# Kernel tuning notes

Measured on AMD Instinct MI355X. Metric: run time of the kernel, lower is better.

Reference implementation:

```python
import jax, jax.numpy as jnp
import numpy as np

DEPTH = 15  # complete binary tree, N = 2**DEPTH - 1 nodes, heap layout


def setup_inputs() -> dict:
    key = jax.random.key(0)
    ks = jax.random.split(key, 9)
    D, H = 512, 512
    N = 2 ** DEPTH - 1
    s = 0.02
    return {
        "x": jax.random.normal(ks[0], (N, D), jnp.float32),
        "Wi": jax.random.normal(ks[1], (H, D + H), jnp.float32) * s,
        "bi": jax.random.normal(ks[2], (H,), jnp.float32) * s,
        "Wf": jax.random.normal(ks[3], (H, D + H), jnp.float32) * s,
        "bf": jax.random.normal(ks[4], (H,), jnp.float32) * s,
        "Wo": jax.random.normal(ks[5], (H, D + H), jnp.float32) * s,
        "bo": jax.random.normal(ks[6], (H,), jnp.float32) * s,
        "Wu": jax.random.normal(ks[7], (H, D + H), jnp.float32) * s,
        "bu": jax.random.normal(ks[8], (H,), jnp.float32) * s,
    }


def _tree_lstm(x, Wi, bi, Wf, bf, Wo, bo, Wu, bu):
    # Child-Sum Tree-LSTM on a complete binary tree in heap layout.
    # Levels processed bottom-up; each level is fully batched.
    N, D = x.shape
    H = Wi.shape[0]
    sig, tanh = jax.nn.sigmoid, jnp.tanh
    h = jnp.zeros((N, H), x.dtype)
    c = jnp.zeros((N, H), x.dtype)
    for lvl in range(DEPTH - 1, -1, -1):
        start = 2 ** lvl - 1
        cnt = 2 ** lvl
        xl = x[start:start + cnt]  # [cnt, D]
        if lvl == DEPTH - 1:
            # leaf_forward: h_children = 0, no forget gates
            xh = jnp.concatenate([xl, jnp.zeros((cnt, H), x.dtype)], axis=1)
            i = sig(xh @ Wi.T + bi)
            o = sig(xh @ Wo.T + bo)
            u = tanh(xh @ Wu.T + bu)
            cl = i * u
        else:
            cs = 2 * start + 1  # first child index of this level
            ch = h[cs:cs + 2 * cnt].reshape(cnt, 2, H)
            cc = c[cs:cs + 2 * cnt].reshape(cnt, 2, H)
            h_l, h_r = ch[:, 0], ch[:, 1]
            hsum = h_l + h_r  # child-sum
            xh = jnp.concatenate([xl, hsum], axis=1)
            i = sig(xh @ Wi.T + bi)
            o = sig(xh @ Wo.T + bo)
            u = tanh(xh @ Wu.T + bu)
            # per-child forget gates: f_k = sigmoid(Wf @ [x; h_k] + bf)
            f_l = sig(jnp.concatenate([xl, h_l], axis=1) @ Wf.T + bf)
            f_r = sig(jnp.concatenate([xl, h_r], axis=1) @ Wf.T + bf)
            cl = i * u + f_l * cc[:, 0] + f_r * cc[:, 1]
        hl = o * tanh(cl)
        h = h.at[start:start + cnt].set(hl)
        c = c.at[start:start + cnt].set(cl)
    return h[0], c[0]  # root (h, c), matching torch forward's return


def reference(x, Wi, bi, Wf, bf, Wo, bo, Wu, bu):
    return _tree_lstm(x, Wi, bi, Wf, bf, Wo, bo, Wu, bu)
```

## Files before the change

### kernel.cpp

```cpp
#include <hip/hip_runtime.h>

typedef __attribute__((ext_vector_type(8))) short bf16x8;
typedef __attribute__((ext_vector_type(4))) float f32x4;

#define HHE 512

__device__ __forceinline__ unsigned short rne_bf16(float f) {
    union { float f; unsigned u; } v; v.f = f;
    unsigned r = v.u + 0x7FFFu + ((v.u >> 16) & 1u);
    return (unsigned short)(r >> 16);
}
__device__ __forceinline__ float bf2f(unsigned short s) {
    union { unsigned u; float f; } v; v.u = ((unsigned)s) << 16; return v.f;
}
__device__ __forceinline__ float sigf(float v)   { return 1.0f / (1.0f + __expf(-v)); }
__device__ __forceinline__ float tanhf_(float v) { return 2.0f / (1.0f + __expf(-2.0f * v)) - 1.0f; }

#define MFMA16(a, b, c) __builtin_amdgcn_mfma_f32_16x16x32_bf16(a, b, c, 0, 0, 0)

#define GLOAD_LDS16(g, l) \
    __builtin_amdgcn_global_load_lds((const __attribute__((address_space(1))) void*)(g), \
                                     (__attribute__((address_space(3))) void*)(l), 16, 0, 0)

__global__ __launch_bounds__(256) void prep(
    const float* __restrict__ x,
    const float* __restrict__ Wi, const float* __restrict__ Wf,
    const float* __restrict__ Wo, const float* __restrict__ Wu,
    unsigned short* __restrict__ xb, unsigned short* __restrict__ wp)
{
    const int b = blockIdx.x;
    if (b < 1024) {
        int t    = b * 256 + threadIdx.x;
        int lane = t & 63;
        int fid  = t >> 6;
        int ks   = fid & 31;
        int jt   = (fid >> 5) & 31;
        int g    = fid >> 10;
        const float* W = (g == 0) ? Wi : (g == 1) ? Wf : (g == 2) ? Wo : Wu;
        int row = jt * 16 + (lane & 15);
        int col = ks * 32 + (lane >> 4) * 8;
        const float* src = W + (size_t)row * 1024 + col;
        float4 f0 = *(const float4*)(src);
        float4 f1 = *(const float4*)(src + 4);
        uint4 o;
        o.x = (unsigned)rne_bf16(f0.x) | ((unsigned)rne_bf16(f0.y) << 16);
        o.y = (unsigned)rne_bf16(f0.z) | ((unsigned)rne_bf16(f0.w) << 16);
        o.z = (unsigned)rne_bf16(f1.x) | ((unsigned)rne_bf16(f1.y) << 16);
        o.w = (unsigned)rne_bf16(f1.z) | ((unsigned)rne_bf16(f1.w) << 16);
        ((uint4*)wp)[t] = o;
    } else {
        size_t idx = (size_t)(b - 1024) * 256 + threadIdx.x;
        if (idx >= 2097088) return;
        const float4* p = (const float4*)x + idx * 2;
        float4 f0 = p[0], f1 = p[1];
        uint4 o;
        o.x = (unsigned)rne_bf16(f0.x) | ((unsigned)rne_bf16(f0.y) << 16);
        o.y = (unsigned)rne_bf16(f0.z) | ((unsigned)rne_bf16(f0.w) << 16);
        o.z = (unsigned)rne_bf16(f1.x) | ((unsigned)rne_bf16(f1.y) << 16);
        o.w = (unsigned)rne_bf16(f1.z) | ((unsigned)rne_bf16(f1.w) << 16);
        ((uint4*)xb)[idx] = o;
    }
}

__global__ __launch_bounds__(256) void leaf_v3(
    const unsigned short* __restrict__ xb, const unsigned short* __restrict__ wp,
    const float* __restrict__ bi, const float* __restrict__ bo, const float* __restrict__ bu,
    unsigned short* __restrict__ hw, unsigned short* __restrict__ cw,
    unsigned short* __restrict__ hso,
    int start, int cnt)
{
    __shared__ __align__(16) unsigned short SH[2 * 2048];

    const int tid  = threadIdx.x;
    const int lane = tid & 63;
    const int wv   = tid >> 6;
    const int q    = lane >> 4;
    const int ln   = lane & 15;
    const int wm   = wv & 1;
    const int wj   = wv >> 1;
    const int mb   = blockIdx.x * 64;
    const int jt0  = blockIdx.y * 4 + wj * 2;

    const int srow   = lane >> 2;
    const int gchunk = (lane & 3) ^ ((lane >> 3) & 3);
    const int stage_row = mb + wv * 16 + srow;
    const int rdoff = ((q ^ ((ln >> 1) & 3)) * 8);

    const unsigned short* wpl = wp + (size_t)lane * 8;

    f32x4 zero = {0.f, 0.f, 0.f, 0.f};
    f32x4 acc_i[2][2], acc_o[2][2], acc_u[2][2];
    #pragma unroll
    for (int t = 0; t < 2; ++t)
        #pragma unroll
        for (int ji = 0; ji < 2; ++ji) {
            acc_i[t][ji] = zero; acc_o[t][ji] = zero; acc_u[t][ji] = zero;
        }

    bf16x8 WA[3][2], WB[3][2];

    auto loadW = [&](bf16x8 (&W)[3][2], int ksabs) {
        #pragma unroll
        for (int g = 0; g < 3; ++g) {
            const int gg = (g == 0) ? 0 : (g + 1);
            #pragma unroll
            for (int ji = 0; ji < 2; ++ji)
                W[g][ji] = *(const bf16x8*)(wpl + ((size_t)((gg * 32 + jt0 + ji) * 32 + ksabs)) * 512);
        }
    };

    loadW(WA, 0);
    {
        const unsigned short* g = xb + (size_t)(start + stage_row) * HHE + gchunk * 8;
        GLOAD_LDS16(g, &SH[0 * 2048 + wv * 512]);
    }
    __syncthreads();

    auto body = [&](int ks, bf16x8 (&WU)[3][2], bf16x8 (&WP)[3][2], int prefks) {
        const int cur = ks & 1;
        if (ks < 15) {
            const unsigned short* g = xb + (size_t)(start + stage_row) * HHE + (ks + 1) * 32 + gchunk * 8;
            GLOAD_LDS16(g, &SH[(cur ^ 1) * 2048 + wv * 512]);
        }
        loadW(WP, prefks);
        bf16x8 a0 = *(const bf16x8*)&SH[cur * 2048 + (wm * 32 + 0 + ln) * 32 + rdoff];
        bf16x8 a1 = *(const bf16x8*)&SH[cur * 2048 + (wm * 32 + 16 + ln) * 32 + rdoff];
        #pragma unroll
        for (int ji = 0; ji < 2; ++ji) {
            acc_i[0][ji] = MFMA16(a0, WU[0][ji], acc_i[0][ji]);
            acc_i[1][ji] = MFMA16(a1, WU[0][ji], acc_i[1][ji]);
            acc_o[0][ji] = MFMA16(a0, WU[1][ji], acc_o[0][ji]);
            acc_o[1][ji] = MFMA16(a1, WU[1][ji], acc_o[1][ji]);
            acc_u[0][ji] = MFMA16(a0, WU[2][ji], acc_u[0][ji]);
            acc_u[1][ji] = MFMA16(a1, WU[2][ji], acc_u[1][ji]);
        }
        __syncthreads();
    };

    for (int kk = 0; kk < 8; ++kk) {
        body(2 * kk,     WA, WB, 2 * kk + 1);
        body(2 * kk + 1, WB, WA, (kk == 7) ? 15 : 2 * kk + 2);
    }

    #pragma unroll
    for (int ji = 0; ji < 2; ++ji) {
        const int jj = (jt0 + ji) * 16 + ln;
        const float bij = bi[jj], boj = bo[jj], buj = bu[jj];
        #pragma unroll
        for (int t = 0; t < 2; ++t) {
            const int n0 = mb + wm * 32 + t * 16 + q * 4;
            float hv[4];
            #pragma unroll
            for (int r = 0; r < 4; ++r) {
                const int node = n0 + r;
                float gi = sigf(acc_i[t][ji][r] + bij);
                float go = sigf(acc_o[t][ji][r] + boj);
                float gu = tanhf_(acc_u[t][ji][r] + buj);
                float cnv = gi * gu;
                float hnv = go * tanhf_(cnv);
                hv[r] = hnv;
                size_t oix = (size_t)node * HHE + jj;
                hw[oix] = rne_bf16(hnv);
                cw[oix] = rne_bf16(cnv);
            }
            hso[(size_t)(n0 >> 1) * HHE + jj]       = rne_bf16(hv[0] + hv[1]);
            hso[(size_t)((n0 >> 1) + 1) * HHE + jj] = rne_bf16(hv[2] + hv[3]);
        }
    }
}

__global__ __launch_bounds__(256) void level_v3(
    const unsigned short* __restrict__ xb, const unsigned short* __restrict__ wp,
    const float* __restrict__ bi, const float* __restrict__ bfv,
    const float* __restrict__ bo, const float* __restrict__ bu,
    const unsigned short* __restrict__ hc, const unsigned short* __restrict__ cc,
    const unsigned short* __restrict__ hs,
    unsigned short* __restrict__ hw, unsigned short* __restrict__ cw,
    unsigned short* __restrict__ hso,
    int start, int cnt)
{
    __shared__ __align__(16) unsigned short SH[2 * 3 * 2048];

    const int tid  = threadIdx.x;
    const int lane = tid & 63;
    const int wv   = tid >> 6;
    const int q    = lane >> 4;
    const int ln   = lane & 15;
    const int wm   = wv & 1;
    const int wj   = wv >> 1;
    const int mb   = blockIdx.x * 64;
    const int jt0  = blockIdx.y * 4 + wj * 2;

    const int srow   = lane >> 2;
    const int gchunk = (lane & 3) ^ ((lane >> 3) & 3);
    const int stage_row = mb + wv * 16 + srow;
    const int rdoff = ((q ^ ((ln >> 1) & 3)) * 8);

    const unsigned short* wpl = wp + (size_t)lane * 8;

    f32x4 zero = {0.f, 0.f, 0.f, 0.f};
    f32x4 acc_i[2][2], acc_f[2][2], acc_o[2][2], acc_u[2][2];
    #pragma unroll
    for (int t = 0; t < 2; ++t)
        #pragma unroll
        for (int ji = 0; ji < 2; ++ji) {
            acc_i[t][ji] = zero; acc_f[t][ji] = zero;
            acc_o[t][ji] = zero; acc_u[t][ji] = zero;
        }

    bf16x8 WA[4][2], WB[4][2];

    auto loadW = [&](bf16x8 (&W)[4][2], int ksabs) {
        #pragma unroll
        for (int g = 0; g < 4; ++g)
            #pragma unroll
            for (int ji = 0; ji < 2; ++ji)
                W[g][ji] = *(const bf16x8*)(wpl + ((size_t)((g * 32 + jt0 + ji) * 32 + ksabs)) * 512);
    };

    loadW(WA, 0);
    {
        const unsigned short* g = xb + (size_t)(start + stage_row) * HHE + gchunk * 8;
        GLOAD_LDS16(g, &SH[(0 * 3 + 0) * 2048 + wv * 512]);
    }
    __syncthreads();

    auto p1_body = [&](int ks, bf16x8 (&WU)[4][2], bf16x8 (&WP)[4][2], int prefks) {
        const int cur = ks & 1;
        if (ks < 15) {
            const unsigned short* g = xb + (size_t)(start + stage_row) * HHE + (ks + 1) * 32 + gchunk * 8;
            GLOAD_LDS16(g, &SH[((cur ^ 1) * 3 + 0) * 2048 + wv * 512]);
        }
        loadW(WP, prefks);
        bf16x8 a0 = *(const bf16x8*)&SH[(cur * 3 + 0) * 2048 + (wm * 32 + 0 + ln) * 32 + rdoff];
        bf16x8 a1 = *(const bf16x8*)&SH[(cur * 3 + 0) * 2048 + (wm * 32 + 16 + ln) * 32 + rdoff];
        #pragma unroll
        for (int ji = 0; ji < 2; ++ji) {
            acc_i[0][ji] = MFMA16(a0, WU[0][ji], acc_i[0][ji]);
            acc_i[1][ji] = MFMA16(a1, WU[0][ji], acc_i[1][ji]);
            acc_f[0][ji] = MFMA16(a0, WU[1][ji], acc_f[0][ji]);
            acc_f[1][ji] = MFMA16(a1, WU[1][ji], acc_f[1][ji]);
            acc_o[0][ji] = MFMA16(a0, WU[2][ji], acc_o[0][ji]);
            acc_o[1][ji] = MFMA16(a1, WU[2][ji], acc_o[1][ji]);
            acc_u[0][ji] = MFMA16(a0, WU[3][ji], acc_u[0][ji]);
            acc_u[1][ji] = MFMA16(a1, WU[3][ji], acc_u[1][ji]);
        }
        __syncthreads();
    };

    for (int kk = 0; kk < 8; ++kk) {
        p1_body(2 * kk,     WA, WB, 2 * kk + 1);
        p1_body(2 * kk + 1, WB, WA, (kk == 7) ? 16 : 2 * kk + 2);
    }

    f32x4 acc_fl[2][2], acc_fr[2][2];
    #pragma unroll
    for (int t = 0; t < 2; ++t)
        #pragma unroll
        for (int ji = 0; ji < 2; ++ji) { acc_fl[t][ji] = acc_f[t][ji]; acc_fr[t][ji] = acc_f[t][ji]; }

    {
        const unsigned short* gs = hs + (size_t)stage_row * HHE + gchunk * 8;
        const unsigned short* gl = hc + ((size_t)(2 * stage_row)) * HHE + gchunk * 8;
        GLOAD_LDS16(gs, &SH[(0 * 3 + 0) * 2048 + wv * 512]);
        GLOAD_LDS16(gl, &SH[(0 * 3 + 1) * 2048 + wv * 512]);
        GLOAD_LDS16(gl + HHE, &SH[(0 * 3 + 2) * 2048 + wv * 512]);
    }
    __syncthreads();

    auto p2_body = [&](int ks, bf16x8 (&WU)[4][2], bf16x8 (&WP)[4][2], int prefks) {
        const int cur = ks & 1;
        if (ks < 15) {
            const unsigned short* gs = hs + (size_t)stage_row * HHE + (ks + 1) * 32 + gchunk * 8;
            const unsigned short* gl = hc + ((size_t)(2 * stage_row)) * HHE + (ks + 1) * 32 + gchunk * 8;
            GLOAD_LDS16(gs, &SH[((cur ^ 1) * 3 + 0) * 2048 + wv * 512]);
            GLOAD_LDS16(gl, &SH[((cur ^ 1) * 3 + 1) * 2048 + wv * 512]);
            GLOAD_LDS16(gl + HHE, &SH[((cur ^ 1) * 3 + 2) * 2048 + wv * 512]);
        }
        loadW(WP, prefks);
        bf16x8 s0 = *(const bf16x8*)&SH[(cur * 3 + 0) * 2048 + (wm * 32 + 0 + ln) * 32 + rdoff];
        bf16x8 s1 = *(const bf16x8*)&SH[(cur * 3 + 0) * 2048 + (wm * 32 + 16 + ln) * 32 + rdoff];
        bf16x8 l0 = *(const bf16x8*)&SH[(cur * 3 + 1) * 2048 + (wm * 32 + 0 + ln) * 32 + rdoff];
        bf16x8 l1 = *(const bf16x8*)&SH[(cur * 3 + 1) * 2048 + (wm * 32 + 16 + ln) * 32 + rdoff];
        bf16x8 r0 = *(const bf16x8*)&SH[(cur * 3 + 2) * 2048 + (wm * 32 + 0 + ln) * 32 + rdoff];
        bf16x8 r1 = *(const bf16x8*)&SH[(cur * 3 + 2) * 2048 + (wm * 32 + 16 + ln) * 32 + rdoff];
        #pragma unroll
        for (int ji = 0; ji < 2; ++ji) {
            acc_i[0][ji]  = MFMA16(s0, WU[0][ji], acc_i[0][ji]);
            acc_i[1][ji]  = MFMA16(s1, WU[0][ji], acc_i[1][ji]);
            acc_o[0][ji]  = MFMA16(s0, WU[2][ji], acc_o[0][ji]);
            acc_o[1][ji]  = MFMA16(s1, WU[2][ji], acc_o[1][ji]);
            acc_u[0][ji]  = MFMA16(s0, WU[3][ji], acc_u[0][ji]);
            acc_u[1][ji]  = MFMA16(s1, WU[3][ji], acc_u[1][ji]);
            acc_fl[0][ji] = MFMA16(l0, WU[1][ji], acc_fl[0][ji]);
            acc_fl[1][ji] = MFMA16(l1, WU[1][ji], acc_fl[1][ji]);
            acc_fr[0][ji] = MFMA16(r0, WU[1][ji], acc_fr[0][ji]);
            acc_fr[1][ji] = MFMA16(r1, WU[1][ji], acc_fr[1][ji]);
        }
        __syncthreads();
    };

    for (int kk = 0; kk < 8; ++kk) {
        p2_body(2 * kk,     WA, WB, 16 + 2 * kk + 1);
        p2_body(2 * kk + 1, WB, WA, (kk == 7) ? 31 : 16 + 2 * kk + 2);
    }

    #pragma unroll
    for (int ji = 0; ji < 2; ++ji) {
        const int jj = (jt0 + ji) * 16 + ln;
        const float bij = bi[jj], bfj = bfv[jj], boj = bo[jj], buj = bu[jj];
        #pragma unroll
        for (int t = 0; t < 2; ++t) {
            const int n0 = mb + wm * 32 + t * 16 + q * 4;
            float hv[4];
            #pragma unroll
            for (int r = 0; r < 4; ++r) {
                const int node = n0 + r;
                size_t cix = (size_t)(2 * node) * HHE + jj;
                float cl = bf2f(cc[cix]);
                float cr = bf2f(cc[cix + HHE]);
                float gi  = sigf(acc_i[t][ji][r] + bij);
                float gfl = sigf(acc_fl[t][ji][r] + bfj);
                float gfr = sigf(acc_fr[t][ji][r] + bfj);
                float go  = sigf(acc_o[t][ji][r] + boj);
                float gu  = tanhf_(acc_u[t][ji][r] + buj);
                float cnv = gi * gu + gfl * cl + gfr * cr;
                float hnv = go * tanhf_(cnv);
                hv[r] = hnv;
                size_t oix = (size_t)node * HHE + jj;
                hw[oix] = rne_bf16(hnv);
                cw[oix] = rne_bf16(cnv);
            }
            hso[(size_t)(n0 >> 1) * HHE + jj]       = rne_bf16(hv[0] + hv[1]);
            hso[(size_t)((n0 >> 1) + 1) * HHE + jj] = rne_bf16(hv[2] + hv[3]);
        }
    }
}

__global__ __launch_bounds__(256) void level_sm(
    const unsigned short* __restrict__ xb, const unsigned short* __restrict__ wp,
    const float* __restrict__ bi, const float* __restrict__ bfv,
    const float* __restrict__ bo, const float* __restrict__ bu,
    const unsigned short* __restrict__ hc, const unsigned short* __restrict__ cc,
    const unsigned short* __restrict__ hs,
    unsigned short* __restrict__ hw, unsigned short* __restrict__ cw,
    unsigned short* __restrict__ hso,
    float* __restrict__ f32out,
    int start, int cnt)
{
    const int tid  = threadIdx.x;
    const int lane = tid & 63;
    const int wv   = tid >> 6;
    const int quad = lane >> 4;
    const int ln   = lane & 15;
    const int mb   = blockIdx.x * 32;
    const int jt   = blockIdx.y * 4 + wv;
    const int j    = jt * 16 + ln;

    int row[2];
    #pragma unroll
    for (int t = 0; t < 2; ++t) {
        int r = mb + t * 16 + ln;
        row[t] = (r < cnt) ? r : (cnt - 1);
    }
    const unsigned short* ax[2];
    #pragma unroll
    for (int t = 0; t < 2; ++t) ax[t] = xb + (size_t)(start + row[t]) * HHE + quad * 8;

    const unsigned short* bw[4];
    #pragma unroll
    for (int g = 0; g < 4; ++g) bw[g] = wp + ((size_t)(g * 32 + jt) * 32) * 512 + lane * 8;

    f32x4 zero = {0.f, 0.f, 0.f, 0.f};
    f32x4 acc_i[2], acc_f[2], acc_o[2], acc_u[2];
    #pragma unroll
    for (int t = 0; t < 2; ++t) { acc_i[t] = zero; acc_f[t] = zero; acc_o[t] = zero; acc_u[t] = zero; }

    #pragma unroll 4
    for (int ks = 0; ks < 16; ++ks) {
        bf16x8 a[2];
        #pragma unroll
        for (int t = 0; t < 2; ++t) { a[t] = *(const bf16x8*)ax[t]; ax[t] += 32; }
        bf16x8 b0 = *(const bf16x8*)bw[0]; bw[0] += 512;
        bf16x8 b1 = *(const bf16x8*)bw[1]; bw[1] += 512;
        bf16x8 b2 = *(const bf16x8*)bw[2]; bw[2] += 512;
        bf16x8 b3 = *(const bf16x8*)bw[3]; bw[3] += 512;
        #pragma unroll
        for (int t = 0; t < 2; ++t) {
            acc_i[t] = MFMA16(a[t], b0, acc_i[t]);
            acc_f[t] = MFMA16(a[t], b1, acc_f[t]);
            acc_o[t] = MFMA16(a[t], b2, acc_o[t]);
            acc_u[t] = MFMA16(a[t], b3, acc_u[t]);
        }
    }

    f32x4 acc_fl[2], acc_fr[2];
    #pragma unroll
    for (int t = 0; t < 2; ++t) { acc_fl[t] = acc_f[t]; acc_fr[t] = acc_f[t]; }

    const unsigned short* as[2];
    const unsigned short* al[2];
    const unsigned short* ar[2];
    #pragma unroll
    for (int t = 0; t < 2; ++t) {
        as[t] = hs + (size_t)row[t] * HHE + quad * 8;
        al[t] = hc + (size_t)(2 * row[t]) * HHE + quad * 8;
        ar[t] = al[t] + HHE;
    }

    #pragma unroll 4
    for (int ks = 0; ks < 16; ++ks) {
        bf16x8 b0 = *(const bf16x8*)bw[0]; bw[0] += 512;
        bf16x8 b1 = *(const bf16x8*)bw[1]; bw[1] += 512;
        bf16x8 b2 = *(const bf16x8*)bw[2]; bw[2] += 512;
        bf16x8 b3 = *(const bf16x8*)bw[3]; bw[3] += 512;
        bf16x8 s[2];
        #pragma unroll
        for (int t = 0; t < 2; ++t) { s[t] = *(const bf16x8*)as[t]; as[t] += 32; }
        #pragma unroll
        for (int t = 0; t < 2; ++t) {
            acc_i[t] = MFMA16(s[t], b0, acc_i[t]);
            acc_o[t] = MFMA16(s[t], b2, acc_o[t]);
            acc_u[t] = MFMA16(s[t], b3, acc_u[t]);
        }
        bf16x8 l[2];
        #pragma unroll
        for (int t = 0; t < 2; ++t) { l[t] = *(const bf16x8*)al[t]; al[t] += 32; }
        #pragma unroll
        for (int t = 0; t < 2; ++t) acc_fl[t] = MFMA16(l[t], b1, acc_fl[t]);
        bf16x8 rr[2];
        #pragma unroll
        for (int t = 0; t < 2; ++t) { rr[t] = *(const bf16x8*)ar[t]; ar[t] += 32; }
        #pragma unroll
        for (int t = 0; t < 2; ++t) acc_fr[t] = MFMA16(rr[t], b1, acc_fr[t]);
    }

    const float bij = bi[j], bfj = bfv[j], boj = bo[j], buj = bu[j];
    #pragma unroll
    for (int t = 0; t < 2; ++t) {
        const int n0 = mb + t * 16 + quad * 4;
        float hv[4];
        #pragma unroll
        for (int r = 0; r < 4; ++r) {
            const int node = n0 + r;
            const int ncl  = (node < cnt) ? node : (cnt - 1);
            size_t cix = (size_t)(2 * ncl) * HHE + j;
            float cl = bf2f(cc[cix]);
            float cr = bf2f(cc[cix + HHE]);
            float gi  = sigf(acc_i[t][r] + bij);
            float gfl = sigf(acc_fl[t][r] + bfj);
            float gfr = sigf(acc_fr[t][r] + bfj);
            float go  = sigf(acc_o[t][r] + boj);
            float gu  = tanhf_(acc_u[t][r] + buj);
            float cnv = gi * gu + gfl * cl + gfr * cr;
            float hnv = go * tanhf_(cnv);
            hv[r] = hnv;
            if (node < cnt) {
                size_t oix = (size_t)node * HHE + j;
                hw[oix] = rne_bf16(hnv);
                cw[oix] = rne_bf16(cnv);
                if (f32out) {
                    f32out[(size_t)node * 1024 + j]       = hnv;
                    f32out[(size_t)node * 1024 + 512 + j] = cnv;
                }
            }
        }
        if (n0 + 1 < cnt) hso[(size_t)(n0 >> 1) * HHE + j]       = rne_bf16(hv[0] + hv[1]);
        if (n0 + 3 < cnt) hso[(size_t)((n0 >> 1) + 1) * HHE + j] = rne_bf16(hv[2] + hv[3]);
    }
}

extern "C" void kernel_launch(void* const* d_in, const int* in_sizes, int n_in,
                              void* d_out, int out_size, void* d_ws, size_t ws_size,
                              hipStream_t stream) {
    const float* x  = (const float*)d_in[0];
    const float* Wi = (const float*)d_in[1];
    const float* bi = (const float*)d_in[2];
    const float* Wf = (const float*)d_in[3];
    const float* bf = (const float*)d_in[4];
    const float* Wo = (const float*)d_in[5];
    const float* bo = (const float*)d_in[6];
    const float* Wu = (const float*)d_in[7];
    const float* bu = (const float*)d_in[8];
    float* out = (float*)d_out;

    unsigned short* xb  = (unsigned short*)d_ws;
    unsigned short* wp  = xb  + 16776704;
    unsigned short* hA  = wp  + 2097152;
    unsigned short* hB  = hA  + 8388608;
    unsigned short* hs1 = hB  + 4194304;
    unsigned short* hs2 = hs1 + 4194304;
    unsigned short* cA  = hs2 + 2097152;
    unsigned short* cB  = cA  + 8388608;

    prep<<<9216, 256, 0, stream>>>(x, Wi, Wf, Wo, Wu, xb, wp);

    leaf_v3<<<dim3(256, 8), 256, 0, stream>>>(xb, wp, bi, bo, bu, hA, cA, hs1, 16383, 16384);

    for (int lvl = 13; lvl >= 6; --lvl) {
        int cnt   = 1 << lvl;
        int start = cnt - 1;
        const unsigned short *hc, *cc, *hs;
        unsigned short *hw, *cw, *hso;
        if (lvl & 1) { hc = hA; cc = cA; hs = hs1; hw = hB; cw = cB; hso = hs2; }
        else         { hc = hB; cc = cB; hs = hs2; hw = hA; cw = cA; hso = hs1; }
        level_v3<<<dim3(cnt / 64, 8), 256, 0, stream>>>(xb, wp, bi, bf, bo, bu,
                                                        hc, cc, hs, hw, cw, hso, start, cnt);
    }

    for (int lvl = 5; lvl >= 0; --lvl) {
        int cnt   = 1 << lvl;
        int start = cnt - 1;
        const unsigned short *hc, *cc, *hs;
        unsigned short *hw, *cw, *hso;
        if (lvl & 1) { hc = hA; cc = cA; hs = hs1; hw = hB; cw = cB; hso = hs2; }
        else         { hc = hB; cc = cB; hs = hs2; hw = hA; cw = cA; hso = hs1; }
        float* f32out = (lvl == 0) ? out : nullptr;
        level_sm<<<dim3((cnt + 31) / 32, 8), 256, 0, stream>>>(xb, wp, bi, bf, bo, bu,
                                                               hc, cc, hs, hw, cw, hso, f32out,
                                                               start, cnt);
    }
}
```

Baseline: 564.2 us.

## Triple-buffer LDS staging with one barrier per k-step and manual vmcnt waits

Switches the leaf and level kernels from double-buffered LDS staging with two __syncthreads per k-step to a three-slot ring buffer. Each step now has a single s_barrier, preceded by explicit s_waitcnt vmcnt counts that let the prefetch of the next slice stay in flight. s_setprio also raises wave priority around the MFMA block. The goal is to remove a barrier per step and overlap global-to-LDS loads with matrix math, at the cost of more LDS and hand-tuned vmcnt counts that break if the compiler reorders or adds memory ops. The leaf kernel computes its slot index with an odd nested expression instead of a modulo.

```diff
diff --git a/kernel.cpp b/kernel.cpp
--- a/kernel.cpp
+++ b/kernel.cpp
@@ -69,7 +69,7 @@
     unsigned short* __restrict__ hso,
     int start, int cnt)
 {
-    __shared__ __align__(16) unsigned short SH[2 * 2048];
+    __shared__ __align__(16) unsigned short SH[3 * 2048];
 
     const int tid  = threadIdx.x;
     const int lane = tid & 63;
@@ -114,17 +114,22 @@
         const unsigned short* g = xb + (size_t)(start + stage_row) * HHE + gchunk * 8;
         GLOAD_LDS16(g, &SH[0 * 2048 + wv * 512]);
     }
-    __syncthreads();
 
     auto body = [&](int ks, bf16x8 (&WU)[3][2], bf16x8 (&WP)[3][2], int prefks) {
-        const int cur = ks & 1;
+        loadW(WP, prefks);
         if (ks < 15) {
+            int nxt = ks + 1; nxt -= (nxt >= 3) ? ((nxt >= 6) ? ((nxt >= 9) ? ((nxt >= 12) ? ((nxt >= 15) ? 15 : 12) : 9) : 6) : 3) : 0;
             const unsigned short* g = xb + (size_t)(start + stage_row) * HHE + (ks + 1) * 32 + gchunk * 8;
-            GLOAD_LDS16(g, &SH[(cur ^ 1) * 2048 + wv * 512]);
-        }
-        loadW(WP, prefks);
+            GLOAD_LDS16(g, &SH[nxt * 2048 + wv * 512]);
+            asm volatile("s_waitcnt vmcnt(7)" ::: "memory");
+        } else {
+            asm volatile("s_waitcnt vmcnt(6)" ::: "memory");
+        }
+        __builtin_amdgcn_s_barrier();
+        int cur = ks % 3;
         bf16x8 a0 = *(const bf16x8*)&SH[cur * 2048 + (wm * 32 + 0 + ln) * 32 + rdoff];
         bf16x8 a1 = *(const bf16x8*)&SH[cur * 2048 + (wm * 32 + 16 + ln) * 32 + rdoff];
+        __builtin_amdgcn_s_setprio(1);
         #pragma unroll
         for (int ji = 0; ji < 2; ++ji) {
             acc_i[0][ji] = MFMA16(a0, WU[0][ji], acc_i[0][ji]);
@@ -134,7 +139,7 @@
             acc_u[0][ji] = MFMA16(a0, WU[2][ji], acc_u[0][ji]);
             acc_u[1][ji] = MFMA16(a1, WU[2][ji], acc_u[1][ji]);
         }
-        __syncthreads();
+        __builtin_amdgcn_s_setprio(0);
     };
 
     for (int kk = 0; kk < 8; ++kk) {
@@ -179,7 +184,7 @@
     unsigned short* __restrict__ hso,
     int start, int cnt)
 {
-    __shared__ __align__(16) unsigned short SH[2 * 3 * 2048];
+    __shared__ __align__(16) unsigned short SH[9 * 2048];
 
     const int tid  = threadIdx.x;
     const int lane = tid & 63;
@@ -223,17 +228,22 @@
         const unsigned short* g = xb + (size_t)(start + stage_row) * HHE + gchunk * 8;
         GLOAD_LDS16(g, &SH[(0 * 3 + 0) * 2048 + wv * 512]);
     }
-    __syncthreads();
 
     auto p1_body = [&](int ks, bf16x8 (&WU)[4][2], bf16x8 (&WP)[4][2], int prefks) {
-        const int cur = ks & 1;
+        loadW(WP, prefks);
         if (ks < 15) {
+            int nxt = (ks + 1) % 3;
             const unsigned short* g = xb + (size_t)(start + stage_row) * HHE + (ks + 1) * 32 + gchunk * 8;
-            GLOAD_LDS16(g, &SH[((cur ^ 1) * 3 + 0) * 2048 + wv * 512]);
-        }
-        loadW(WP, prefks);
+            GLOAD_LDS16(g, &SH[(nxt * 3 + 0) * 2048 + wv * 512]);
+            asm volatile("s_waitcnt vmcnt(9)" ::: "memory");
+        } else {
+            asm volatile("s_waitcnt vmcnt(8)" ::: "memory");
+        }
+        __builtin_amdgcn_s_barrier();
+        int cur = ks % 3;
         bf16x8 a0 = *(const bf16x8*)&SH[(cur * 3 + 0) * 2048 + (wm * 32 + 0 + ln) * 32 + rdoff];
         bf16x8 a1 = *(const bf16x8*)&SH[(cur * 3 + 0) * 2048 + (wm * 32 + 16 + ln) * 32 + rdoff];
+        __builtin_amdgcn_s_setprio(1);
         #pragma unroll
         for (int ji = 0; ji < 2; ++ji) {
             acc_i[0][ji] = MFMA16(a0, WU[0][ji], acc_i[0][ji]);
@@ -245,7 +255,7 @@
             acc_u[0][ji] = MFMA16(a0, WU[3][ji], acc_u[0][ji]);
             acc_u[1][ji] = MFMA16(a1, WU[3][ji], acc_u[1][ji]);
         }
-        __syncthreads();
+        __builtin_amdgcn_s_setprio(0);
     };
 
     for (int kk = 0; kk < 8; ++kk) {
@@ -259,6 +269,7 @@
         #pragma unroll
         for (int ji = 0; ji < 2; ++ji) { acc_fl[t][ji] = acc_f[t][ji]; acc_fr[t][ji] = acc_f[t][ji]; }
 
+    __builtin_amdgcn_s_barrier();
     {
         const unsigned short* gs = hs + (size_t)stage_row * HHE + gchunk * 8;
         const unsigned short* gl = hc + ((size_t)(2 * stage_row)) * HHE + gchunk * 8;
@@ -266,24 +277,29 @@
         GLOAD_LDS16(gl, &SH[(0 * 3 + 1) * 2048 + wv * 512]);
         GLOAD_LDS16(gl + HHE, &SH[(0 * 3 + 2) * 2048 + wv * 512]);
     }
-    __syncthreads();
 
     auto p2_body = [&](int ks, bf16x8 (&WU)[4][2], bf16x8 (&WP)[4][2], int prefks) {
-        const int cur = ks & 1;
+        loadW(WP, prefks);
         if (ks < 15) {
+            int nxt = (ks + 1) % 3;
             const unsigned short* gs = hs + (size_t)stage_row * HHE + (ks + 1) * 32 + gchunk * 8;
             const unsigned short* gl = hc + ((size_t)(2 * stage_row)) * HHE + (ks + 1) * 32 + gchunk * 8;
-            GLOAD_LDS16(gs, &SH[((cur ^ 1) * 3 + 0) * 2048 + wv * 512]);
-            GLOAD_LDS16(gl, &SH[((cur ^ 1) * 3 + 1) * 2048 + wv * 512]);
-            GLOAD_LDS16(gl + HHE, &SH[((cur ^ 1) * 3 + 2) * 2048 + wv * 512]);
-        }
-        loadW(WP, prefks);
+            GLOAD_LDS16(gs, &SH[(nxt * 3 + 0) * 2048 + wv * 512]);
+            GLOAD_LDS16(gl, &SH[(nxt * 3 + 1) * 2048 + wv * 512]);
+            GLOAD_LDS16(gl + HHE, &SH[(nxt * 3 + 2) * 2048 + wv * 512]);
+            asm volatile("s_waitcnt vmcnt(11)" ::: "memory");
+        } else {
+            asm volatile("s_waitcnt vmcnt(8)" ::: "memory");
+        }
+        __builtin_amdgcn_s_barrier();
+        int cur = ks % 3;
         bf16x8 s0 = *(const bf16x8*)&SH[(cur * 3 + 0) * 2048 + (wm * 32 + 0 + ln) * 32 + rdoff];
         bf16x8 s1 = *(const bf16x8*)&SH[(cur * 3 + 0) * 2048 + (wm * 32 + 16 + ln) * 32 + rdoff];
         bf16x8 l0 = *(const bf16x8*)&SH[(cur * 3 + 1) * 2048 + (wm * 32 + 0 + ln) * 32 + rdoff];
         bf16x8 l1 = *(const bf16x8*)&SH[(cur * 3 + 1) * 2048 + (wm * 32 + 16 + ln) * 32 + rdoff];
         bf16x8 r0 = *(const bf16x8*)&SH[(cur * 3 + 2) * 2048 + (wm * 32 + 0 + ln) * 32 + rdoff];
         bf16x8 r1 = *(const bf16x8*)&SH[(cur * 3 + 2) * 2048 + (wm * 32 + 16 + ln) * 32 + rdoff];
+        __builtin_amdgcn_s_setprio(1);
         #pragma unroll
         for (int ji = 0; ji < 2; ++ji) {
             acc_i[0][ji]  = MFMA16(s0, WU[0][ji], acc_i[0][ji]);
@@ -297,7 +313,7 @@
             acc_fr[0][ji] = MFMA16(r0, WU[1][ji], acc_fr[0][ji]);
             acc_fr[1][ji] = MFMA16(r1, WU[1][ji], acc_fr[1][ji]);
         }
-        __syncthreads();
+        __builtin_amdgcn_s_setprio(0);
     };
 
     for (int kk = 0; kk < 8; ++kk) {
```

Result: no change. 574.3 us (+1.8%).

## Fuse top seven tree levels into one persistent kernel with grid barrier

Applied to the files above, without the earlier changes.

Replaces the seven separate launches for levels 6 to 0 with one persistent kernel of 32 blocks. Each block owns 16 hidden columns and keeps its slice of all four gate weight matrices in LDS for every level. Levels are separated by a global atomic spin barrier whose counter is reset in the prep kernel. This removes launch overhead and repeated weight loads on the small, latency-bound top levels, but it relies on all 32 blocks being co-resident and on device-scope fences to make each level's outputs visible to the next.

```diff
diff --git a/kernel.cpp b/kernel.cpp
--- a/kernel.cpp
+++ b/kernel.cpp
@@ -26,11 +26,13 @@
     const float* __restrict__ x,
     const float* __restrict__ Wi, const float* __restrict__ Wf,
     const float* __restrict__ Wo, const float* __restrict__ Wu,
-    unsigned short* __restrict__ xb, unsigned short* __restrict__ wp)
+    unsigned short* __restrict__ xb, unsigned short* __restrict__ wp,
+    int* __restrict__ bar)
 {
     const int b = blockIdx.x;
     if (b < 1024) {
         int t    = b * 256 + threadIdx.x;
+        if (bar && t == 0) *bar = 0;
         int lane = t & 63;
         int fid  = t >> 6;
         int ks   = fid & 31;
@@ -470,6 +472,133 @@
     }
 }
 
+#define TAIL_NBLK 32
+
+__device__ __forceinline__ void tailbar(int* bar, int target) {
+    __syncthreads();
+    if (threadIdx.x == 0) {
+        __threadfence();
+        __hip_atomic_fetch_add(bar, 1, __ATOMIC_RELAXED, __HIP_MEMORY_SCOPE_AGENT);
+        while (__hip_atomic_load(bar, __ATOMIC_RELAXED, __HIP_MEMORY_SCOPE_AGENT) < target)
+            __builtin_amdgcn_s_sleep(2);
+        __threadfence();
+    }
+    __syncthreads();
+}
+
+__global__ __launch_bounds__(256) void tail_fused(
+    const unsigned short* __restrict__ xb, const unsigned short* __restrict__ wp,
+    const float* __restrict__ bi, const float* __restrict__ bfv,
+    const float* __restrict__ bo, const float* __restrict__ bu,
+    unsigned short* __restrict__ hA, unsigned short* __restrict__ cA,
+    unsigned short* __restrict__ hB, unsigned short* __restrict__ cB,
+    unsigned short* __restrict__ hs1, unsigned short* __restrict__ hs2,
+    float* __restrict__ out, int* __restrict__ bar)
+{
+    __shared__ __align__(16) unsigned short WL[128 * 512];
+
+    const int tid  = threadIdx.x;
+    const int lane = tid & 63;
+    const int wv   = tid >> 6;
+    const int quad = lane >> 4;
+    const int ln   = lane & 15;
+    const int jt   = blockIdx.x;
+    const int j    = jt * 16 + ln;
+    const int wl   = lane * 8;
+
+    #pragma unroll
+    for (int i = 0; i < 32; ++i) {
+        int f = i * 4 + wv;
+        const unsigned short* src = wp + ((size_t)(((f >> 5) * 32 + jt) * 32 + (f & 31))) * 512 + lane * 8;
+        GLOAD_LDS16(src, &WL[f * 512]);
+    }
+    __syncthreads();
+
+    const float bij = bi[j], bfj = bfv[j], boj = bo[j], buj = bu[j];
+
+    int k = 0;
+    for (int lvl = 6; lvl >= 0; --lvl) {
+        const int cnt = 1 << lvl;
+        const int start = cnt - 1;
+        const unsigned short *hc, *cc, *hs;
+        unsigned short *hw, *cw, *hso;
+        if (lvl & 1) { hc = hA; cc = cA; hs = hs1; hw = hB; cw = cB; hso = hs2; }
+        else         { hc = hB; cc = cB; hs = hs2; hw = hA; cw = cA; hso = hs1; }
+
+        const int r0  = wv * 16 + ln;
+        const int row = (r0 < cnt) ? r0 : (cnt - 1);
+
+        f32x4 zero = {0.f, 0.f, 0.f, 0.f};
+        f32x4 acc_i = zero, acc_f = zero, acc_o = zero, acc_u = zero;
+
+        const unsigned short* ax = xb + (size_t)(start + row) * HHE + quad * 8;
+        #pragma unroll 4
+        for (int ks = 0; ks < 16; ++ks) {
+            bf16x8 a  = *(const bf16x8*)ax; ax += 32;
+            bf16x8 w0 = *(const bf16x8*)&WL[(0 * 32 + ks) * 512 + wl];
+            bf16x8 w1 = *(const bf16x8*)&WL[(1 * 32 + ks) * 512 + wl];
+            bf16x8 w2 = *(const bf16x8*)&WL[(2 * 32 + ks) * 512 + wl];
+            bf16x8 w3 = *(const bf16x8*)&WL[(3 * 32 + ks) * 512 + wl];
+            acc_i = MFMA16(a, w0, acc_i);
+            acc_f = MFMA16(a, w1, acc_f);
+            acc_o = MFMA16(a, w2, acc_o);
+            acc_u = MFMA16(a, w3, acc_u);
+        }
+
+        f32x4 acc_fl = acc_f, acc_fr = acc_f;
+        const unsigned short* as = hs + (size_t)row * HHE + quad * 8;
+        const unsigned short* al = hc + (size_t)(2 * row) * HHE + quad * 8;
+        const unsigned short* ar = al + HHE;
+        #pragma unroll 4
+        for (int ks = 0; ks < 16; ++ks) {
+            bf16x8 w0 = *(const bf16x8*)&WL[(0 * 32 + 16 + ks) * 512 + wl];
+            bf16x8 w1 = *(const bf16x8*)&WL[(1 * 32 + 16 + ks) * 512 + wl];
+            bf16x8 w2 = *(const bf16x8*)&WL[(2 * 32 + 16 + ks) * 512 + wl];
+            bf16x8 w3 = *(const bf16x8*)&WL[(3 * 32 + 16 + ks) * 512 + wl];
+            bf16x8 s  = *(const bf16x8*)as; as += 32;
+            bf16x8 l  = *(const bf16x8*)al; al += 32;
+            bf16x8 rr = *(const bf16x8*)ar; ar += 32;
+            acc_i  = MFMA16(s,  w0, acc_i);
+            acc_o  = MFMA16(s,  w2, acc_o);
+            acc_u  = MFMA16(s,  w3, acc_u);
+            acc_fl = MFMA16(l,  w1, acc_fl);
+            acc_fr = MFMA16(rr, w1, acc_fr);
+        }
+
+        const int n0 = wv * 16 + quad * 4;
+        float hv[4];
+        #pragma unroll
+        for (int r = 0; r < 4; ++r) {
+            const int node = n0 + r;
+            const int ncl  = (node < cnt) ? node : (cnt - 1);
+            size_t cix = (size_t)(2 * ncl) * HHE + j;
+            float cl = bf2f(cc[cix]);
+            float cr = bf2f(cc[cix + HHE]);
+            float gi  = sigf(acc_i[r] + bij);
+            float gfl = sigf(acc_fl[r] + bfj);
+            float gfr = sigf(acc_fr[r] + bfj);
+            float go  = sigf(acc_o[r] + boj);
+            float gu  = tanhf_(acc_u[r] + buj);
+            float cnv = gi * gu + gfl * cl + gfr * cr;
+            float hnv = go * tanhf_(cnv);
+            hv[r] = hnv;
+            if (node < cnt) {
+                size_t oix = (size_t)node * HHE + j;
+                hw[oix] = rne_bf16(hnv);
+                cw[oix] = rne_bf16(cnv);
+                if (lvl == 0) {
+                    out[(size_t)node * 1024 + j]       = hnv;
+                    out[(size_t)node * 1024 + 512 + j] = cnv;
+                }
+            }
+        }
+        if (n0 + 1 < cnt) hso[(size_t)(n0 >> 1) * HHE + j]       = rne_bf16(hv[0] + hv[1]);
+        if (n0 + 3 < cnt) hso[(size_t)((n0 >> 1) + 1) * HHE + j] = rne_bf16(hv[2] + hv[3]);
+
+        if (lvl > 0) { ++k; tailbar(bar, TAIL_NBLK * k); }
+    }
+}
+
 extern "C" void kernel_launch(void* const* d_in, const int* in_sizes, int n_in,
                               void* d_out, int out_size, void* d_ws, size_t ws_size,
                               hipStream_t stream) {
@@ -493,11 +622,15 @@
     unsigned short* cA  = hs2 + 2097152;
     unsigned short* cB  = cA  + 8388608;
 
-    prep<<<9216, 256, 0, stream>>>(x, Wi, Wf, Wo, Wu, xb, wp);
+    const size_t BAR_OFF = (size_t)96 << 20;
+    const bool fused = ws_size >= BAR_OFF + 64;
+    int* bar = (int*)((char*)d_ws + BAR_OFF);
+
+    prep<<<9216, 256, 0, stream>>>(x, Wi, Wf, Wo, Wu, xb, wp, fused ? bar : nullptr);
 
     leaf_v3<<<dim3(256, 8), 256, 0, stream>>>(xb, wp, bi, bo, bu, hA, cA, hs1, 16383, 16384);
 
-    for (int lvl = 13; lvl >= 6; --lvl) {
+    for (int lvl = 13; lvl >= 7; --lvl) {
         int cnt   = 1 << lvl;
         int start = cnt - 1;
         const unsigned short *hc, *cc, *hs;
@@ -508,16 +641,23 @@
                                                         hc, cc, hs, hw, cw, hso, start, cnt);
     }
 
-    for (int lvl = 5; lvl >= 0; --lvl) {
-        int cnt   = 1 << lvl;
-        int start = cnt - 1;
-        const unsigned short *hc, *cc, *hs;
-        unsigned short *hw, *cw, *hso;
-        if (lvl & 1) { hc = hA; cc = cA; hs = hs1; hw = hB; cw = cB; hso = hs2; }
-        else         { hc = hB; cc = cB; hs = hs2; hw = hA; cw = cA; hso = hs1; }
-        float* f32out = (lvl == 0) ? out : nullptr;
-        level_sm<<<dim3((cnt + 31) / 32, 8), 256, 0, stream>>>(xb, wp, bi, bf, bo, bu,
-                                                               hc, cc, hs, hw, cw, hso, f32out,
-                                                               start, cnt);
-    }
-}
+    if (fused) {
+        tail_fused<<<TAIL_NBLK, 256, 0, stream>>>(xb, wp, bi, bf, bo, bu,
+                                                  hA, cA, hB, cB, hs1, hs2, out, bar);
+    } else {
+        level_v3<<<dim3(1, 8), 256, 0, stream>>>(xb, wp, bi, bf, bo, bu,
+                                                 hB, cB, hs2, hA, cA, hs1, 63, 64);
+        for (int lvl = 5; lvl >= 0; --lvl) {
+            int cnt   = 1 << lvl;
+            int start = cnt - 1;
+            const unsigned short *hc, *cc, *hs;
+            unsigned short *hw, *cw, *hso;
+            if (lvl & 1) { hc = hA; cc = cA; hs = hs1; hw = hB; cw = cB; hso = hs2; }
+            else         { hc = hB; cc = cB; hs = hs2; hw = hA; cw = cA; hso = hs1; }
+            float* f32out = (lvl == 0) ? out : nullptr;
+            level_sm<<<dim3((cnt + 31) / 32, 8), 256, 0, stream>>>(xb, wp, bi, bf, bo, bu,
+                                                                   hc, cc, hs, hw, cw, hso, f32out,
+                                                                   start, cnt);
+        }
+    }
+}
```

After: 517.8 us. 1.09x faster.
